# Performance work log

Measured on AMD Instinct MI355X. Metric: run time of the kernel, lower is better.

Reference implementation:

```python
import jax, jax.numpy as jnp
import numpy as np

EPS = 1e-6
HQ, HKV, HD = 16, 4, 64   # num_q_heads, num_kv_heads, head_dim
TOPK = 2                  # num_exp_tokens
B, S, H, E, I = 2, 1024, 1024, 8, 2048


def _rms(x, w):
    return x * jax.lax.rsqrt(jnp.mean(x * x, -1, keepdims=True) + EPS) * w


def _rope(x, cos, sin):
    # x: [B,S,h,D]; cos/sin: [S,D/2]
    x1, x2 = jnp.split(x, 2, axis=-1)
    c = cos[None, :, None, :]
    s = sin[None, :, None, :]
    return jnp.concatenate([x1 * c - x2 * s, x1 * s + x2 * c], axis=-1)


def setup_inputs() -> dict:
    key = jax.random.key(0)
    ks = jax.random.split(key, 12)
    w = lambda k, sh: jax.random.normal(k, sh, jnp.float32) * 0.02
    return {
        "x": jax.random.normal(ks[0], (B, S, H), jnp.float32),
        "freq": jax.random.uniform(ks[1], (S, HD // 2), jnp.float32) * 6.28,
        "norm1_w": jnp.ones((H,), jnp.float32),
        "norm2_w": jnp.ones((H,), jnp.float32),
        "wq": w(ks[2], (H, HQ * HD)),
        "wk": w(ks[3], (H, HKV * HD)),
        "wv": w(ks[4], (H, HKV * HD)),
        "wo": w(ks[5], (HQ * HD, H)),
        "qn_w": jnp.ones((HD,), jnp.float32),
        "kn_w": jnp.ones((HD,), jnp.float32),
        "gate_w": w(ks[6], (H, E)),
        "w1": w(ks[7], (E, H, I)),
        "w2": w(ks[8], (E, I, H)),
        "w3": w(ks[9], (E, H, I)),
    }


def reference(x, freq, norm1_w, norm2_w, wq, wk, wv, wo, qn_w, kn_w,
              gate_w, w1, w2, w3):
    b, s, h = x.shape
    # ---- GQA attention with qk_norm + RoPE ----
    hn = _rms(x, norm1_w)
    q = (hn @ wq).reshape(b, s, HQ, HD)
    k = (hn @ wk).reshape(b, s, HKV, HD)
    v = (hn @ wv).reshape(b, s, HKV, HD)
    q = _rms(q, qn_w)
    k = _rms(k, kn_w)
    cos, sin = jnp.cos(freq), jnp.sin(freq)
    q = _rope(q, cos, sin)
    k = _rope(k, cos, sin)
    rep = HQ // HKV
    kr = jnp.repeat(k, rep, axis=2)  # [b,s,HQ,HD]
    vr = jnp.repeat(v, rep, axis=2)
    scores = jnp.einsum('bqhd,bkhd->bhqk', q, kr) * (HD ** -0.5)
    mask = jnp.tril(jnp.ones((s, s), bool))
    scores = jnp.where(mask, scores, jnp.finfo(scores.dtype).min)
    att = jax.nn.softmax(scores, axis=-1)
    y = jnp.einsum('bhqk,bkhd->bqhd', att, vr).reshape(b, s, HQ * HD) @ wo
    x = x + y

    # ---- Sparse MoE FFN (top-k softmax gate, SwiGLU experts) ----
    t = _rms(x, norm2_w).reshape(b * s, h)
    probs = jax.nn.softmax(t @ gate_w, axis=-1)          # [T,E]
    vals, idx = jax.lax.top_k(probs, TOPK)               # [T,k]
    vals = vals / jnp.sum(vals, -1, keepdims=True)       # renormalize top-k
    T = b * s
    combine = jnp.zeros((T, E), t.dtype).at[
        jnp.arange(T)[:, None], idx].add(vals)           # [T,E]
    u = jnp.einsum('th,ehi->eti', t, w1)
    g = jax.nn.silu(u) * jnp.einsum('th,ehi->eti', t, w3)
    ye = jnp.einsum('eti,eih->eth', g, w2)               # [E,T,H]
    moe = jnp.einsum('eth,te->th', ye, combine).reshape(b, s, h)
    return (x + moe, k, v)
```

## Files before the change

kernel.cpp:

```cpp
#include <hip/hip_runtime.h>
#include <hip/hip_bf16.h>

#define HQn 16
#define HKVn 4
#define HDn 64
#define Bn 2
#define Sn 1024
#define Hn 1024
#define En 8
#define In 2048
#define Tn 2048
#define EPSf 1e-6f

typedef __attribute__((ext_vector_type(8))) short bf16x8;
typedef __attribute__((ext_vector_type(4))) float f32x4;

__device__ __forceinline__ unsigned short f2bf(float f) {
  unsigned u = __float_as_uint(f);
  u += 0x7fffu + ((u >> 16) & 1u);
  return (unsigned short)(u >> 16);
}
__device__ __forceinline__ float bf2f(unsigned short u) {
  return __uint_as_float(((unsigned)u) << 16);
}
__device__ __forceinline__ void gll16(const void* g, void* l) {
  __builtin_amdgcn_global_load_lds(
      (const __attribute__((address_space(1))) void*)g,
      (__attribute__((address_space(3))) void*)l, 16, 0, 0);
}

__global__ __launch_bounds__(256) void k_tcvt(
    const float* __restrict__ src, unsigned short* __restrict__ dst,
    int R, int C, size_t sZ, size_t dZ) {
  src += (size_t)blockIdx.z * sZ;
  dst += (size_t)blockIdx.z * dZ;
  int c0 = blockIdx.x * 64, r0 = blockIdx.y * 64;
  __shared__ float t[64][65];
  int tid = threadIdx.x;
  int lr = tid >> 4, lc = (tid & 15) * 4;
#pragma unroll
  for (int p = 0; p < 4; p++) {
    float4 v = *(const float4*)(src + (size_t)(r0 + lr + p * 16) * C + c0 + lc);
    t[lr + p * 16][lc + 0] = v.x; t[lr + p * 16][lc + 1] = v.y;
    t[lr + p * 16][lc + 2] = v.z; t[lr + p * 16][lc + 3] = v.w;
  }
  __syncthreads();
  int oc = tid >> 2;
  int seg = (tid & 3) * 16;
  unsigned pk[8];
#pragma unroll
  for (int j = 0; j < 8; j++) {
    unsigned short lo = f2bf(t[seg + 2 * j][oc]);
    unsigned short hi = f2bf(t[seg + 2 * j + 1][oc]);
    pk[j] = (unsigned)lo | ((unsigned)hi << 16);
  }
  uint4* dp = (uint4*)(dst + (size_t)(c0 + oc) * R + r0 + seg);
  dp[0] = make_uint4(pk[0], pk[1], pk[2], pk[3]);
  dp[1] = make_uint4(pk[4], pk[5], pk[6], pk[7]);
}

__global__ __launch_bounds__(256) void k_tcvt2(
    const float* __restrict__ src, unsigned short* __restrict__ dsth,
    unsigned short* __restrict__ dstl, int R, int C) {
  int c0 = blockIdx.x * 64, r0 = blockIdx.y * 64;
  __shared__ float t[64][65];
  int tid = threadIdx.x;
  int lr = tid >> 4, lc = (tid & 15) * 4;
#pragma unroll
  for (int p = 0; p < 4; p++) {
    float4 v = *(const float4*)(src + (size_t)(r0 + lr + p * 16) * C + c0 + lc);
    t[lr + p * 16][lc + 0] = v.x; t[lr + p * 16][lc + 1] = v.y;
    t[lr + p * 16][lc + 2] = v.z; t[lr + p * 16][lc + 3] = v.w;
  }
  __syncthreads();
  int oc = tid >> 2;
  int seg = (tid & 3) * 16;
  unsigned pkh[8], pkl[8];
#pragma unroll
  for (int j = 0; j < 8; j++) {
    float a = t[seg + 2 * j][oc], b = t[seg + 2 * j + 1][oc];
    unsigned short ahh = f2bf(a), bhh = f2bf(b);
    unsigned short alo = f2bf(a - bf2f(ahh)), blo = f2bf(b - bf2f(bhh));
    pkh[j] = (unsigned)ahh | ((unsigned)bhh << 16);
    pkl[j] = (unsigned)alo | ((unsigned)blo << 16);
  }
  size_t db = (size_t)(c0 + oc) * R + r0 + seg;
  uint4* dph = (uint4*)(dsth + db);
  dph[0] = make_uint4(pkh[0], pkh[1], pkh[2], pkh[3]);
  dph[1] = make_uint4(pkh[4], pkh[5], pkh[6], pkh[7]);
  uint4* dpl = (uint4*)(dstl + db);
  dpl[0] = make_uint4(pkl[0], pkl[1], pkl[2], pkl[3]);
  dpl[1] = make_uint4(pkl[4], pkl[5], pkl[6], pkl[7]);
}

__global__ __launch_bounds__(256) void k_rmsnorm(
    const float* __restrict__ x, const float* __restrict__ w,
    unsigned short* __restrict__ outh, unsigned short* __restrict__ outl) {
  int row = blockIdx.x, tid = threadIdx.x;
  size_t off = (size_t)row * Hn + tid * 4;
  float4 v = *(const float4*)(x + off);
  float ss = v.x * v.x + v.y * v.y + v.z * v.z + v.w * v.w;
#pragma unroll
  for (int o = 32; o > 0; o >>= 1) ss += __shfl_xor(ss, o);
  __shared__ float ls[4];
  if ((tid & 63) == 0) ls[tid >> 6] = ss;
  __syncthreads();
  float tot = ls[0] + ls[1] + ls[2] + ls[3];
  float sc = rsqrtf(tot * (1.0f / Hn) + EPSf);
  float4 wv = *(const float4*)(w + tid * 4);
  float o0 = v.x * sc * wv.x, o1 = v.y * sc * wv.y;
  float o2 = v.z * sc * wv.z, o3 = v.w * sc * wv.w;
  ushort4 h4, l4;
  h4.x = f2bf(o0); l4.x = f2bf(o0 - bf2f(h4.x));
  h4.y = f2bf(o1); l4.y = f2bf(o1 - bf2f(h4.y));
  h4.z = f2bf(o2); l4.z = f2bf(o2 - bf2f(h4.z));
  h4.w = f2bf(o3); l4.w = f2bf(o3 - bf2f(h4.w));
  *(ushort4*)(outh + off) = h4;
  *(ushort4*)(outl + off) = l4;
}

__global__ __launch_bounds__(256) void k_resid_norm(
    const float* __restrict__ x, const float* __restrict__ y,
    const float* __restrict__ w, float* __restrict__ x2out,
    float* __restrict__ tout, unsigned short* __restrict__ tbf) {
  int row = blockIdx.x, tid = threadIdx.x;
  size_t off = (size_t)row * Hn + tid * 4;
  float4 xv = *(const float4*)(x + off);
  float4 yv = *(const float4*)(y + off);
  float4 s;
  s.x = xv.x + yv.x; s.y = xv.y + yv.y; s.z = xv.z + yv.z; s.w = xv.w + yv.w;
  *(float4*)(x2out + off) = s;
  float ss = s.x * s.x + s.y * s.y + s.z * s.z + s.w * s.w;
#pragma unroll
  for (int o = 32; o > 0; o >>= 1) ss += __shfl_xor(ss, o);
  __shared__ float ls[4];
  if ((tid & 63) == 0) ls[tid >> 6] = ss;
  __syncthreads();
  float tot = ls[0] + ls[1] + ls[2] + ls[3];
  float sc = rsqrtf(tot * (1.0f / Hn) + EPSf);
  float4 wv4 = *(const float4*)(w + tid * 4);
  float4 t4;
  t4.x = s.x * sc * wv4.x; t4.y = s.y * sc * wv4.y;
  t4.z = s.z * sc * wv4.z; t4.w = s.w * sc * wv4.w;
  *(float4*)(tout + off) = t4;
  ushort4 b4;
  b4.x = f2bf(t4.x); b4.y = f2bf(t4.y); b4.z = f2bf(t4.z); b4.w = f2bf(t4.w);
  *(ushort4*)(tbf + off) = b4;
}

template<int MT>
__global__ __launch_bounds__(256) void k_pgemm(
    const unsigned short* __restrict__ Ah, const unsigned short* __restrict__ Al,
    const unsigned short* __restrict__ Bth, const unsigned short* __restrict__ Btl,
    float* __restrict__ C, int N, int K) {
  constexpr int BM = MT * 32;
  constexpr int ASL = BM * 32;
  __shared__ __align__(16) short smAh[2][ASL], smAl[2][ASL];
  __shared__ __align__(16) short smBh[2][4096], smBl[2][4096];
  int tid = threadIdx.x, wave = tid >> 6, lane = tid & 63;
  int n0 = blockIdx.x * 128, m0 = blockIdx.y * BM;
  int wm = wave >> 1, wn = wave & 1;
  int r0 = ((tid >> 6) << 4) | (tid & 15);
  int k0 = ((tid >> 4) & 3) * 8;
  int r1 = r0 + 64;
  const unsigned short* pAh0 = Ah + (size_t)(m0 + r0) * K + k0;
  const unsigned short* pAl0 = Al + (size_t)(m0 + r0) * K + k0;
  const unsigned short* pBh0 = Bth + (size_t)(n0 + r0) * K + k0;
  const unsigned short* pBl0 = Btl + (size_t)(n0 + r0) * K + k0;
  const unsigned short* pBh1 = Bth + (size_t)(n0 + r1) * K + k0;
  const unsigned short* pBl1 = Btl + (size_t)(n0 + r1) * K + k0;
  const unsigned short* pAh1 = pAh0;
  const unsigned short* pAl1 = pAl0;
  if constexpr (MT == 4) {
    pAh1 = Ah + (size_t)(m0 + r1) * K + k0;
    pAl1 = Al + (size_t)(m0 + r1) * K + k0;
  }
  int d0 = tid * 8, d1 = (256 + tid) * 8;
  auto STAGE = [&](int b, int kb) {
    gll16(pAh0 + kb, &smAh[b][d0]);
    gll16(pAl0 + kb, &smAl[b][d0]);
    if constexpr (MT == 4) {
      gll16(pAh1 + kb, &smAh[b][d1]);
      gll16(pAl1 + kb, &smAl[b][d1]);
    }
    gll16(pBh0 + kb, &smBh[b][d0]);
    gll16(pBl0 + kb, &smBl[b][d0]);
    gll16(pBh1 + kb, &smBh[b][d1]);
    gll16(pBl1 + kb, &smBl[b][d1]);
  };
  f32x4 zf = {0.f, 0.f, 0.f, 0.f};
  f32x4 acc[MT][4];
#pragma unroll
  for (int i = 0; i < MT; i++)
#pragma unroll
    for (int j = 0; j < 4; j++) acc[i][j] = zf;
  STAGE(0, 0);
  __syncthreads();
  for (int kb = 0; kb < K; kb += 32) {
    int cur = (kb >> 5) & 1;
    if (kb + 32 < K) STAGE(cur ^ 1, kb + 32);
    bf16x8 ah[MT], al[MT], bh[4], bl[4];
#pragma unroll
    for (int i = 0; i < MT; i++) {
      ah[i] = *(const bf16x8*)&smAh[cur][((wm * MT + i) * 64 + lane) * 8];
      al[i] = *(const bf16x8*)&smAl[cur][((wm * MT + i) * 64 + lane) * 8];
    }
#pragma unroll
    for (int j = 0; j < 4; j++) {
      bh[j] = *(const bf16x8*)&smBh[cur][((wn * 4 + j) * 64 + lane) * 8];
      bl[j] = *(const bf16x8*)&smBl[cur][((wn * 4 + j) * 64 + lane) * 8];
    }
#pragma unroll
    for (int i = 0; i < MT; i++)
#pragma unroll
      for (int j = 0; j < 4; j++) {
        acc[i][j] = __builtin_amdgcn_mfma_f32_16x16x32_bf16(ah[i], bh[j], acc[i][j], 0, 0, 0);
        acc[i][j] = __builtin_amdgcn_mfma_f32_16x16x32_bf16(ah[i], bl[j], acc[i][j], 0, 0, 0);
        acc[i][j] = __builtin_amdgcn_mfma_f32_16x16x32_bf16(al[i], bh[j], acc[i][j], 0, 0, 0);
      }
    __syncthreads();
  }
  int cr = (lane >> 4) * 4, cc = lane & 15;
#pragma unroll
  for (int i = 0; i < MT; i++) {
    int row0 = m0 + (wm * MT + i) * 16 + cr;
#pragma unroll
    for (int j = 0; j < 4; j++) {
      int col = n0 + (wn * 4 + j) * 16 + cc;
#pragma unroll
      for (int r = 0; r < 4; r++)
        C[(size_t)(row0 + r) * N + col] = acc[i][j][r];
    }
  }
}

__global__ __launch_bounds__(256) void k_qkv_post(
    const float* __restrict__ qkv, const float* __restrict__ qn_w,
    const float* __restrict__ kn_w, const float* __restrict__ freq,
    float* __restrict__ q_t,
    unsigned short* __restrict__ kT8h, unsigned short* __restrict__ kT8l,
    unsigned short* __restrict__ vT8h, unsigned short* __restrict__ vT8l,
    float* __restrict__ k_out, float* __restrict__ v_out) {
  int gw = blockIdx.x * 4 + (threadIdx.x >> 6);
  int lane = threadIdx.x & 63;
  int token = gw / 24;
  int hh = gw % 24;
  int b = token / Sn, s = token % Sn;
  if (hh >= 20) {
    int h = hh - 20;
    float v = qkv[(size_t)token * 1536 + 1280 + h * HDn + lane];
    unsigned short hi = f2bf(v);
    unsigned short lo = f2bf(v - bf2f(hi));
    size_t vb = (((size_t)(b * HKVn + h) * 128 + (s >> 3)) * 64 + lane) * 8 + (s & 7);
    vT8h[vb] = hi; vT8l[vb] = lo;
    v_out[(size_t)token * (HKVn * HDn) + h * HDn + lane] = v;
    return;
  }
  bool isq = hh < 16;
  int h = isq ? hh : hh - 16;
  float val = isq ? qkv[(size_t)token * 1536 + h * HDn + lane]
                  : qkv[(size_t)token * 1536 + 1024 + h * HDn + lane];
  float ss = val * val;
#pragma unroll
  for (int o = 32; o > 0; o >>= 1) ss += __shfl_xor(ss, o);
  float scn = rsqrtf(ss * (1.0f / HDn) + EPSf);
  float w = isq ? qn_w[lane] : kn_w[lane];
  float xn = val * scn * w;
  float f = freq[(size_t)s * (HDn / 2) + (lane & 31)];
  float c = cosf(f), sn = sinf(f);
  float partner = __shfl_xor(xn, 32);
  float out = (lane < 32) ? (xn * c - partner * sn) : (partner * sn + xn * c);
  if (isq) {
    q_t[(((size_t)(b * HQn + h)) * Sn + s) * HDn + lane] = out;
  } else {
    unsigned short hi = f2bf(out);
    unsigned short lo = f2bf(out - bf2f(hi));
    size_t kb = (((size_t)(b * HKVn + h) * 8 + (lane >> 3)) * Sn + s) * 8 + (lane & 7);
    kT8h[kb] = hi; kT8l[kb] = lo;
    k_out[(size_t)token * (HKVn * HDn) + h * HDn + lane] = out;
  }
}

__global__ __launch_bounds__(256) void k_attn_mfma(
    const float* __restrict__ q_t,
    const unsigned short* __restrict__ kT8h, const unsigned short* __restrict__ kT8l,
    const unsigned short* __restrict__ vT8h, const unsigned short* __restrict__ vT8l,
    unsigned short* __restrict__ yh, unsigned short* __restrict__ yl) {
  __shared__ __align__(16) unsigned short klh[4096], kll[4096];
  __shared__ __align__(16) unsigned short vth[4096], vtl[4096];
  __shared__ __align__(16) unsigned short Ph[4][1152], Pl[4][1152];
  int bid = blockIdx.x;
  int qt = 63 - (bid & 63);
  int kvh = (bid >> 6) & 3;
  int b = bid >> 8;
  int tid = threadIdx.x, w = tid >> 6, lane = tid & 63;
  int h = kvh * 4 + w;
  int g = lane >> 4, li = lane & 15;
  const float* qrow = q_t + (((size_t)(b * HQn + h) * Sn) + qt * 16 + li) * HDn + g * 8;
  bf16x8 qh[2], ql[2];
#pragma unroll
  for (int kc = 0; kc < 2; kc++) {
    float v[8];
    *(float4*)(v) = *(const float4*)(qrow + kc * 32);
    *(float4*)(v + 4) = *(const float4*)(qrow + kc * 32 + 4);
#pragma unroll
    for (int j = 0; j < 8; j++) {
      unsigned short hi = f2bf(v[j]);
      qh[kc][j] = (short)hi;
      ql[kc][j] = (short)f2bf(v[j] - bf2f(hi));
    }
  }
  size_t bh = (size_t)(b * HKVn + kvh) * 65536;
  f32x4 acc[4];
  f32x4 zf = {0.f, 0.f, 0.f, 0.f};
#pragma unroll
  for (int nt = 0; nt < 4; nt++) acc[nt] = zf;
  float m_[4] = {-1e30f, -1e30f, -1e30f, -1e30f};
  float l_[4] = {0.f, 0.f, 0.f, 0.f};
  int rowb = qt * 16 + g * 4;
  int kmax = qt * 16 + 15;
  for (int kk = 0; kk <= kmax; kk += 64) {
    __syncthreads();
#pragma unroll
    for (int i = 0; i < 2; i++) {
      int idx = w * 2 + i;
      gll16(kT8h + bh + (size_t)idx * 8192 + (size_t)kk * 8 + lane * 8, &klh[idx * 512]);
      gll16(kT8l + bh + (size_t)idx * 8192 + (size_t)kk * 8 + lane * 8, &kll[idx * 512]);
      gll16(vT8h + bh + (size_t)(kk / 8 + idx) * 512 + lane * 8, &vth[idx * 512]);
      gll16(vT8l + bh + (size_t)(kk / 8 + idx) * 512 + lane * 8, &vtl[idx * 512]);
    }
    __syncthreads();
    f32x4 st[4];
#pragma unroll
    for (int kt = 0; kt < 4; kt++) st[kt] = zf;
#pragma unroll
    for (int kt = 0; kt < 4; kt++)
#pragma unroll
      for (int kc = 0; kc < 2; kc++) {
        int ko = (kc * 4 + g) * 512 + (kt * 16 + li) * 8;
        bf16x8 kh = *(const bf16x8*)&klh[ko];
        bf16x8 klo = *(const bf16x8*)&kll[ko];
        st[kt] = __builtin_amdgcn_mfma_f32_16x16x32_bf16(qh[kc], kh, st[kt], 0, 0, 0);
        st[kt] = __builtin_amdgcn_mfma_f32_16x16x32_bf16(qh[kc], klo, st[kt], 0, 0, 0);
        st[kt] = __builtin_amdgcn_mfma_f32_16x16x32_bf16(ql[kc], kh, st[kt], 0, 0, 0);
      }
    float mx[4] = {-1e30f, -1e30f, -1e30f, -1e30f};
#pragma unroll
    for (int kt = 0; kt < 4; kt++) {
      int key = kk + kt * 16 + li;
#pragma unroll
      for (int r = 0; r < 4; r++) {
        float s = st[kt][r] * 0.125f;
        if (key > rowb + r) s = -1e30f;
        st[kt][r] = s;
        mx[r] = fmaxf(mx[r], s);
      }
    }
#pragma unroll
    for (int r = 0; r < 4; r++) {
#pragma unroll
      for (int o = 1; o < 16; o <<= 1) mx[r] = fmaxf(mx[r], __shfl_xor(mx[r], o));
      float mn = fmaxf(m_[r], mx[r]);
      mx[r] = __expf(m_[r] - mn);
      m_[r] = mn;
    }
    float rs[4] = {0.f, 0.f, 0.f, 0.f};
#pragma unroll
    for (int kt = 0; kt < 4; kt++)
#pragma unroll
      for (int r = 0; r < 4; r++) {
        float p = __expf(st[kt][r] - m_[r]);
        rs[r] += p;
        unsigned short phh = f2bf(p);
        Ph[w][(g * 4 + r) * 72 + kt * 16 + li] = phh;
        Pl[w][(g * 4 + r) * 72 + kt * 16 + li] = f2bf(p - bf2f(phh));
      }
#pragma unroll
    for (int r = 0; r < 4; r++) {
#pragma unroll
      for (int o = 1; o < 16; o <<= 1) rs[r] += __shfl_xor(rs[r], o);
      l_[r] = l_[r] * mx[r] + rs[r];
#pragma unroll
      for (int nt = 0; nt < 4; nt++) acc[nt][r] *= mx[r];
    }
    bf16x8 pfh[2], pfl[2];
#pragma unroll
    for (int kc = 0; kc < 2; kc++) {
      int po = li * 72 + kc * 32 + g * 8;
      pfh[kc] = *(const bf16x8*)&Ph[w][po];
      pfl[kc] = *(const bf16x8*)&Pl[w][po];
    }
#pragma unroll
    for (int nt = 0; nt < 4; nt++)
#pragma unroll
      for (int kc = 0; kc < 2; kc++) {
        int vo = (kc * 4 + g) * 512 + (nt * 16 + li) * 8;
        bf16x8 vh = *(const bf16x8*)&vth[vo];
        bf16x8 vl = *(const bf16x8*)&vtl[vo];
        acc[nt] = __builtin_amdgcn_mfma_f32_16x16x32_bf16(pfh[kc], vh, acc[nt], 0, 0, 0);
        acc[nt] = __builtin_amdgcn_mfma_f32_16x16x32_bf16(pfh[kc], vl, acc[nt], 0, 0, 0);
        acc[nt] = __builtin_amdgcn_mfma_f32_16x16x32_bf16(pfl[kc], vh, acc[nt], 0, 0, 0);
      }
  }
  size_t ybase = ((size_t)(b * Sn) + qt * 16) * (HQn * HDn) + h * HDn;
#pragma unroll
  for (int r = 0; r < 4; r++) {
    float inv = 1.f / l_[r];
#pragma unroll
    for (int nt = 0; nt < 4; nt++) {
      size_t idx = ybase + (size_t)(g * 4 + r) * (HQn * HDn) + nt * 16 + li;
      float v = acc[nt][r] * inv;
      unsigned short hi = f2bf(v);
      yh[idx] = hi;
      yl[idx] = f2bf(v - bf2f(hi));
    }
  }
}

__global__ __launch_bounds__(256) void k_router(
    const float* __restrict__ t, const float* __restrict__ gw_,
    int* __restrict__ idx, float* __restrict__ val, int* __restrict__ cnt) {
  int tok = blockIdx.x * 4 + (threadIdx.x >> 6);
  int lane = threadIdx.x & 63;
  const float* tr = t + (size_t)tok * Hn;
  float s[8] = {0, 0, 0, 0, 0, 0, 0, 0};
  for (int hh = lane; hh < Hn; hh += 64) {
    float tv = tr[hh];
    float4 g0 = *(const float4*)(gw_ + hh * 8);
    float4 g1 = *(const float4*)(gw_ + hh * 8 + 4);
    s[0] = fmaf(tv, g0.x, s[0]); s[1] = fmaf(tv, g0.y, s[1]);
    s[2] = fmaf(tv, g0.z, s[2]); s[3] = fmaf(tv, g0.w, s[3]);
    s[4] = fmaf(tv, g1.x, s[4]); s[5] = fmaf(tv, g1.y, s[5]);
    s[6] = fmaf(tv, g1.z, s[6]); s[7] = fmaf(tv, g1.w, s[7]);
  }
#pragma unroll
  for (int e = 0; e < 8; e++)
#pragma unroll
    for (int off = 32; off > 0; off >>= 1) s[e] += __shfl_xor(s[e], off);
  if (lane == 0) {
    float mx = s[0];
    for (int e = 1; e < 8; e++) mx = fmaxf(mx, s[e]);
    float p[8];
    for (int e = 0; e < 8; e++) p[e] = __expf(s[e] - mx);
    int e0 = 0;
    for (int e = 1; e < 8; e++) if (p[e] > p[e0]) e0 = e;
    int e1 = (e0 == 0) ? 1 : 0;
    for (int e = 0; e < 8; e++) if (e != e0 && p[e] > p[e1]) e1 = e;
    float v0 = p[e0], v1 = p[e1], inv = 1.f / (v0 + v1);
    idx[tok * 2] = e0; idx[tok * 2 + 1] = e1;
    val[tok * 2] = v0 * inv; val[tok * 2 + 1] = v1 * inv;
    atomicAdd(&cnt[e0], 1); atomicAdd(&cnt[e1], 1);
  }
}

__global__ void k_scan(const int* __restrict__ cnt, int* __restrict__ offs,
                       int* __restrict__ cursor) {
  if (threadIdx.x == 0) {
    int run = 0;
    for (int e = 0; e < En; e++) { offs[e] = run; cursor[e] = run; run += cnt[e]; }
  }
}

__global__ __launch_bounds__(256) void k_scatter(
    const int* __restrict__ idx, const float* __restrict__ val,
    int* __restrict__ cursor, int* __restrict__ tokl, float* __restrict__ wvl) {
  int t = blockIdx.x * 256 + threadIdx.x;
#pragma unroll
  for (int slot = 0; slot < 2; slot++) {
    int e = idx[t * 2 + slot];
    int pos = atomicAdd(&cursor[e], 1);
    tokl[pos] = t;
    wvl[pos] = val[t * 2 + slot];
  }
}

__global__ __launch_bounds__(256) void k_gather(
    const unsigned short* __restrict__ tb, const int* __restrict__ tokl,
    unsigned short* __restrict__ tg) {
  int r = blockIdx.x;
  int tk = tokl[r];
  const ushort4* s = (const ushort4*)(tb + (size_t)tk * Hn);
  ushort4* d = (ushort4*)(tg + (size_t)r * Hn);
  d[threadIdx.x] = s[threadIdx.x];
}

__global__ __launch_bounds__(512) void k_moe13(
    const unsigned short* __restrict__ tg, const unsigned short* __restrict__ w13t,
    unsigned short* __restrict__ ug, const int* __restrict__ cnt,
    const int* __restrict__ offs) {
  int e = blockIdx.z;
  int n_e = cnt[e];
  int mt = blockIdx.y;
  if (mt * 256 >= n_e) return;
  int base = offs[e];
  const unsigned short* A = tg + (size_t)(base + mt * 256) * Hn;
  const unsigned short* Bt = w13t + (size_t)e * (2 * In) * Hn;
  __shared__ __align__(16) short smA[2][8192];
  __shared__ __align__(16) short smB[2][4096];
  int tid = threadIdx.x;
  int wave = tid >> 6, lane = tid & 63;
  int n0 = blockIdx.x * 128;
  int wm = wave >> 1, wn = wave & 1;
  int r0s = ((tid >> 6) << 4) | (tid & 15);
  int k0s = ((tid >> 4) & 3) * 8;
  const unsigned short* ApA = A + (size_t)r0s * Hn + k0s;
  const unsigned short* ApB = A + (size_t)(r0s + 128) * Hn + k0s;
  const unsigned short* BpB = Bt + (size_t)(n0 + r0s) * Hn + k0s;
  auto STAGE = [&](int b, int kb) {
    gll16(ApA + kb, &smA[b][tid * 8]);
    gll16(ApB + kb, &smA[b][(512 + tid) * 8]);
    gll16(BpB + kb, &smB[b][tid * 8]);
  };
  f32x4 zf = {0.f, 0.f, 0.f, 0.f};
  f32x4 acc[4][4];
#pragma unroll
  for (int i = 0; i < 4; i++)
#pragma unroll
    for (int j = 0; j < 4; j++) acc[i][j] = zf;
  STAGE(0, 0);
  __syncthreads();
  for (int kb = 0; kb < Hn; kb += 32) {
    int cur = (kb >> 5) & 1;
    if (kb + 32 < Hn) STAGE(cur ^ 1, kb + 32);
    bf16x8 af[4], bfr[4];
#pragma unroll
    for (int i = 0; i < 4; i++)
      af[i] = *(const bf16x8*)&smA[cur][((wm * 4 + i) * 64 + lane) * 8];
#pragma unroll
    for (int j = 0; j < 4; j++)
      bfr[j] = *(const bf16x8*)&smB[cur][((wn * 4 + j) * 64 + lane) * 8];
#pragma unroll
    for (int i = 0; i < 4; i++)
#pragma unroll
      for (int j = 0; j < 4; j++)
        acc[i][j] = __builtin_amdgcn_mfma_f32_16x16x32_bf16(af[i], bfr[j], acc[i][j], 0, 0, 0);
    __syncthreads();
  }
  int cr = (lane >> 4) * 4, cc = lane & 15;
#pragma unroll
  for (int i = 0; i < 4; i++) {
    int lrow0 = wm * 64 + i * 16 + cr;
#pragma unroll
    for (int j = 0; j < 4; j++) {
      int ncol = n0 + wn * 64 + j * 16 + cc;
#pragma unroll
      for (int r = 0; r < 4; r++) {
        int rr = mt * 256 + lrow0 + r;
        if (rr < n_e)
          ug[(size_t)(base + rr) * (2 * In) + ncol] = f2bf(acc[i][j][r]);
      }
    }
  }
}

__global__ __launch_bounds__(256) void k_act(
    const unsigned short* __restrict__ ug, unsigned short* __restrict__ act) {
  size_t p = ((size_t)blockIdx.x * 256 + threadIdx.x) * 8;
  size_t r = p >> 11;
  int c = (int)(p & 2047);
  const ushort4* up = (const ushort4*)(ug + r * 4096 + c);
  const ushort4* gp = (const ushort4*)(ug + r * 4096 + 2048 + c);
  ushort4* ap = (ushort4*)(act + r * 2048 + c);
#pragma unroll
  for (int h = 0; h < 2; h++) {
    ushort4 uu = up[h], gg = gp[h];
    ushort4 oo;
    float u0 = bf2f(uu.x), u1 = bf2f(uu.y), u2 = bf2f(uu.z), u3 = bf2f(uu.w);
    oo.x = f2bf(u0 / (1.f + __expf(-u0)) * bf2f(gg.x));
    oo.y = f2bf(u1 / (1.f + __expf(-u1)) * bf2f(gg.y));
    oo.z = f2bf(u2 / (1.f + __expf(-u2)) * bf2f(gg.z));
    oo.w = f2bf(u3 / (1.f + __expf(-u3)) * bf2f(gg.w));
    ap[h] = oo;
  }
}

__global__ __launch_bounds__(512) void k_moe2(
    const unsigned short* __restrict__ act, const unsigned short* __restrict__ w2t,
    const int* __restrict__ cnt, const int* __restrict__ offs,
    const int* __restrict__ tokl, const float* __restrict__ wvl,
    float* __restrict__ out0) {
  int e = blockIdx.z;
  int n_e = cnt[e];
  int mt = blockIdx.y;
  if (mt * 128 >= n_e) return;
  int base = offs[e];
  __shared__ int ltok[128];
  __shared__ float lwv[128];
  int tid = threadIdx.x;
  if (tid < 128) {
    int rr = mt * 128 + tid;
    bool v = rr < n_e;
    ltok[tid] = v ? tokl[base + rr] : -1;
    lwv[tid] = v ? wvl[base + rr] : 0.f;
  }
  const unsigned short* A = act + (size_t)(base + mt * 128) * In;
  const unsigned short* Bt = w2t + (size_t)e * Hn * In;
  __shared__ __align__(16) short smA[2][4096];
  __shared__ __align__(16) short smB[2][4096];
  int wave = tid >> 6, lane = tid & 63;
  int n0 = blockIdx.x * 128;
  int wm = wave >> 1, wn = wave & 1;
  int r0s = ((tid >> 6) << 4) | (tid & 15);
  int k0s = ((tid >> 4) & 3) * 8;
  const unsigned short* ApA = A + (size_t)r0s * In + k0s;
  const unsigned short* BpB = Bt + (size_t)(n0 + r0s) * In + k0s;
  auto STAGE = [&](int b, int kb) {
    gll16(ApA + kb, &smA[b][tid * 8]);
    gll16(BpB + kb, &smB[b][tid * 8]);
  };
  f32x4 zf = {0.f, 0.f, 0.f, 0.f};
  f32x4 acc[2][4];
#pragma unroll
  for (int i = 0; i < 2; i++)
#pragma unroll
    for (int j = 0; j < 4; j++) acc[i][j] = zf;
  STAGE(0, 0);
  __syncthreads();
  for (int kb = 0; kb < In; kb += 32) {
    int cur = (kb >> 5) & 1;
    if (kb + 32 < In) STAGE(cur ^ 1, kb + 32);
    bf16x8 af[2], bfr[4];
#pragma unroll
    for (int i = 0; i < 2; i++)
      af[i] = *(const bf16x8*)&smA[cur][((wm * 2 + i) * 64 + lane) * 8];
#pragma unroll
    for (int j = 0; j < 4; j++)
      bfr[j] = *(const bf16x8*)&smB[cur][((wn * 4 + j) * 64 + lane) * 8];
#pragma unroll
    for (int i = 0; i < 2; i++)
#pragma unroll
      for (int j = 0; j < 4; j++)
        acc[i][j] = __builtin_amdgcn_mfma_f32_16x16x32_bf16(af[i], bfr[j], acc[i][j], 0, 0, 0);
    __syncthreads();
  }
  int cr = (lane >> 4) * 4, cc = lane & 15;
#pragma unroll
  for (int i = 0; i < 2; i++) {
    int lrow0 = wm * 32 + i * 16 + cr;
#pragma unroll
    for (int j = 0; j < 4; j++) {
      int ncol = n0 + wn * 64 + j * 16 + cc;
#pragma unroll
      for (int r = 0; r < 4; r++) {
        int lrow = lrow0 + r;
        int tk = ltok[lrow];
        if (tk >= 0)
          atomicAdd(out0 + (size_t)tk * Hn + ncol, lwv[lrow] * acc[i][j][r]);
      }
    }
  }
}

extern "C" void kernel_launch(void* const* d_in, const int* in_sizes, int n_in,
                              void* d_out, int out_size, void* d_ws, size_t ws_size,
                              hipStream_t stream) {
  (void)in_sizes; (void)n_in; (void)out_size; (void)ws_size;
  const float* x      = (const float*)d_in[0];
  const float* freq   = (const float*)d_in[1];
  const float* n1w    = (const float*)d_in[2];
  const float* n2w    = (const float*)d_in[3];
  const float* wq     = (const float*)d_in[4];
  const float* wk     = (const float*)d_in[5];
  const float* wvp    = (const float*)d_in[6];
  const float* wo     = (const float*)d_in[7];
  const float* qn_w   = (const float*)d_in[8];
  const float* kn_w   = (const float*)d_in[9];
  const float* gate_w = (const float*)d_in[10];
  const float* w1     = (const float*)d_in[11];
  const float* w2     = (const float*)d_in[12];
  const float* w3     = (const float*)d_in[13];

  float* out0  = (float*)d_out;
  float* k_out = out0 + (size_t)Tn * Hn;
  float* v_out = k_out + (size_t)Tn * HKVn * HDn;

  char* wsb = (char*)d_ws;
  unsigned short* w13t = (unsigned short*)(wsb + 0);
  unsigned short* w2t  = (unsigned short*)(wsb + 67108864);
  unsigned short* tbf  = (unsigned short*)(wsb + 100663296);
  unsigned short* tg   = (unsigned short*)(wsb + 104857600);
  unsigned short* wqkvt_h = (unsigned short*)(wsb + 113246208);
  unsigned short* wqkvt_l = (unsigned short*)(wsb + 116391936);
  unsigned short* wot_h   = (unsigned short*)(wsb + 119537664);
  unsigned short* wot_l   = (unsigned short*)(wsb + 121634816);
  unsigned short* act  = (unsigned short*)(wsb + 113246208);
  unsigned short* hnh  = (unsigned short*)(wsb + 130023424);
  unsigned short* hnl  = (unsigned short*)(wsb + 134217728);
  float* qkv_raw = (float*)(wsb + 138412032);
  float* q_t   = (float*)(wsb + 150994944);
  unsigned short* kT8h = (unsigned short*)(wsb + 159383552);
  unsigned short* kT8l = (unsigned short*)(wsb + 160432128);
  unsigned short* vT8h = (unsigned short*)(wsb + 161480704);
  unsigned short* vT8l = (unsigned short*)(wsb + 162529280);
  unsigned short* ug = (unsigned short*)(wsb + 130023424);
  unsigned short* yh = (unsigned short*)(wsb + 163577856);
  unsigned short* yl = (unsigned short*)(wsb + 167772160);
  float* y2    = (float*)(wsb + 171966464);
  float* t_norm = (float*)(wsb + 150994944);
  char*  rtr   = wsb + 180355072;
  int*   idxb   = (int*)(rtr);
  float* valb   = (float*)(rtr + 16384);
  int*   cnt    = (int*)(rtr + 32768);
  int*   offs   = (int*)(rtr + 32768 + 128);
  int*   cursor = (int*)(rtr + 32768 + 256);
  int*   tokl   = (int*)(rtr + 32768 + 384);
  float* wvl    = (float*)(rtr + 32768 + 384 + 16384);

  k_tcvt<<<dim3(32, 16, 8), 256, 0, stream>>>(w1, w13t, 1024, 2048,
                                              (size_t)1024 * 2048, (size_t)4096 * 1024);
  k_tcvt<<<dim3(32, 16, 8), 256, 0, stream>>>(w3, w13t + (size_t)2048 * 1024, 1024, 2048,
                                              (size_t)1024 * 2048, (size_t)4096 * 1024);
  k_tcvt<<<dim3(16, 32, 8), 256, 0, stream>>>(w2, w2t, 2048, 1024,
                                              (size_t)2048 * 1024, (size_t)1024 * 2048);
  k_tcvt2<<<dim3(16, 16), 256, 0, stream>>>(wq, wqkvt_h, wqkvt_l, 1024, 1024);
  k_tcvt2<<<dim3(4, 16), 256, 0, stream>>>(wk, wqkvt_h + (size_t)1024 * 1024,
                                           wqkvt_l + (size_t)1024 * 1024, 1024, 256);
  k_tcvt2<<<dim3(4, 16), 256, 0, stream>>>(wvp, wqkvt_h + (size_t)1280 * 1024,
                                           wqkvt_l + (size_t)1280 * 1024, 1024, 256);
  k_tcvt2<<<dim3(16, 16), 256, 0, stream>>>(wo, wot_h, wot_l, 1024, 1024);

  hipMemsetAsync(cnt, 0, 8 * sizeof(int), stream);

  k_rmsnorm<<<Tn, 256, 0, stream>>>(x, n1w, hnh, hnl);
  k_pgemm<4><<<dim3(12, 16), 256, 0, stream>>>(hnh, hnl, wqkvt_h, wqkvt_l,
                                               qkv_raw, 1536, 1024);
  k_qkv_post<<<(Tn * 24) / 4, 256, 0, stream>>>(qkv_raw, qn_w, kn_w,
                                                freq, q_t, kT8h, kT8l, vT8h, vT8l,
                                                k_out, v_out);
  k_attn_mfma<<<Bn * HKVn * 64, 256, 0, stream>>>(q_t, kT8h, kT8l, vT8h, vT8l, yh, yl);
  k_pgemm<2><<<dim3(8, 32), 256, 0, stream>>>(yh, yl, wot_h, wot_l, y2, 1024, 1024);
  k_resid_norm<<<Tn, 256, 0, stream>>>(x, y2, n2w, out0, t_norm, tbf);
  k_router<<<Tn / 4, 256, 0, stream>>>(t_norm, gate_w, idxb, valb, cnt);
  k_scan<<<1, 64, 0, stream>>>(cnt, offs, cursor);
  k_scatter<<<Tn / 256, 256, 0, stream>>>(idxb, valb, cursor, tokl, wvl);
  k_gather<<<2 * Tn, 256, 0, stream>>>(tbf, tokl, tg);
  k_moe13<<<dim3(32, 8, 8), 512, 0, stream>>>(tg, w13t, ug, cnt, offs);
  k_act<<<4096, 256, 0, stream>>>(ug, act);
  k_moe2<<<dim3(8, 16, 8), 512, 0, stream>>>(act, w2t, cnt, offs, tokl, wvl, out0);
}
```

Measured before the change: 680.6 us.

## Enlarge MoE w1/w3 GEMM tile to 256x256 with K=64 double-buffered stages

The expert up-projection GEMM now computes a 256x256 output tile per block instead of 256x128, with each wave owning 128x64. Each pipeline stage loads 64 K-elements instead of 32, through two named shared buffers, and the grid along N is halved. This raises arithmetic intensity and halves the number of barriers per K step. The cost is 128KB of LDS and 128 accumulator registers per thread, which lowers occupancy, and fewer blocks run when experts get few tokens.

```diff
diff --git a/kernel.cpp b/kernel.cpp
--- a/kernel.cpp
+++ b/kernel.cpp
@@ -493,53 +493,70 @@
   int mt = blockIdx.y;
   if (mt * 256 >= n_e) return;
   int base = offs[e];
+  int n0 = blockIdx.x * 256;
   const unsigned short* A = tg + (size_t)(base + mt * 256) * Hn;
-  const unsigned short* Bt = w13t + (size_t)e * (2 * In) * Hn;
-  __shared__ __align__(16) short smA[2][8192];
-  __shared__ __align__(16) short smB[2][4096];
+  const unsigned short* Bt = w13t + (size_t)e * (2 * In) * Hn + (size_t)n0 * Hn;
+  __shared__ __align__(16) short sA0[16384], sA1[16384];
+  __shared__ __align__(16) short sB0[16384], sB1[16384];
   int tid = threadIdx.x;
   int wave = tid >> 6, lane = tid & 63;
-  int n0 = blockIdx.x * 128;
-  int wm = wave >> 1, wn = wave & 1;
-  int r0s = ((tid >> 6) << 4) | (tid & 15);
-  int k0s = ((tid >> 4) & 3) * 8;
-  const unsigned short* ApA = A + (size_t)r0s * Hn + k0s;
-  const unsigned short* ApB = A + (size_t)(r0s + 128) * Hn + k0s;
-  const unsigned short* BpB = Bt + (size_t)(n0 + r0s) * Hn + k0s;
-  auto STAGE = [&](int b, int kb) {
-    gll16(ApA + kb, &smA[b][tid * 8]);
-    gll16(ApB + kb, &smA[b][(512 + tid) * 8]);
-    gll16(BpB + kb, &smB[b][tid * 8]);
-  };
+  int wm = wave >> 2, wn = wave & 3;
+  int rowLo = ((tid >> 6) << 4) | (tid & 15);
+  int kLo = ((tid >> 4) & 3) * 8;
+  const unsigned short* a0 = A + (size_t)rowLo * Hn + kLo;
+  const unsigned short* a1 = A + (size_t)(rowLo + 128) * Hn + kLo;
+  const unsigned short* b0 = Bt + (size_t)rowLo * Hn + kLo;
+  const unsigned short* b1 = Bt + (size_t)(rowLo + 128) * Hn + kLo;
+  size_t d0 = (size_t)tid * 8;
+#define M13_STAGE(S, kb) do { \
+    gll16(a0 + (kb), sA##S + d0); \
+    gll16(a1 + (kb), sA##S + 4096 + d0); \
+    gll16(a0 + (kb) + 32, sA##S + 8192 + d0); \
+    gll16(a1 + (kb) + 32, sA##S + 12288 + d0); \
+    gll16(b0 + (kb), sB##S + d0); \
+    gll16(b1 + (kb), sB##S + 4096 + d0); \
+    gll16(b0 + (kb) + 32, sB##S + 8192 + d0); \
+    gll16(b1 + (kb) + 32, sB##S + 12288 + d0); \
+  } while (0)
+#define M13_COMP(S) do { \
+    _Pragma("unroll") \
+    for (int kk = 0; kk < 2; kk++) { \
+      bf16x8 af[8], bfr[4]; \
+      _Pragma("unroll") \
+      for (int i = 0; i < 8; i++) \
+        af[i] = *(const bf16x8*)(sA##S + kk * 8192 + ((wm * 8 + i) * 64 + lane) * 8); \
+      _Pragma("unroll") \
+      for (int j = 0; j < 4; j++) \
+        bfr[j] = *(const bf16x8*)(sB##S + kk * 8192 + ((wn * 4 + j) * 64 + lane) * 8); \
+      _Pragma("unroll") \
+      for (int i = 0; i < 8; i++) \
+        _Pragma("unroll") \
+        for (int j = 0; j < 4; j++) \
+          acc[i][j] = __builtin_amdgcn_mfma_f32_16x16x32_bf16(af[i], bfr[j], acc[i][j], 0, 0, 0); \
+    } \
+  } while (0)
   f32x4 zf = {0.f, 0.f, 0.f, 0.f};
-  f32x4 acc[4][4];
-#pragma unroll
-  for (int i = 0; i < 4; i++)
+  f32x4 acc[8][4];
+#pragma unroll
+  for (int i = 0; i < 8; i++)
 #pragma unroll
     for (int j = 0; j < 4; j++) acc[i][j] = zf;
-  STAGE(0, 0);
+  M13_STAGE(0, 0);
   __syncthreads();
-  for (int kb = 0; kb < Hn; kb += 32) {
-    int cur = (kb >> 5) & 1;
-    if (kb + 32 < Hn) STAGE(cur ^ 1, kb + 32);
-    bf16x8 af[4], bfr[4];
-#pragma unroll
-    for (int i = 0; i < 4; i++)
-      af[i] = *(const bf16x8*)&smA[cur][((wm * 4 + i) * 64 + lane) * 8];
-#pragma unroll
-    for (int j = 0; j < 4; j++)
-      bfr[j] = *(const bf16x8*)&smB[cur][((wn * 4 + j) * 64 + lane) * 8];
-#pragma unroll
-    for (int i = 0; i < 4; i++)
-#pragma unroll
-      for (int j = 0; j < 4; j++)
-        acc[i][j] = __builtin_amdgcn_mfma_f32_16x16x32_bf16(af[i], bfr[j], acc[i][j], 0, 0, 0);
+  for (int kb = 0; kb < Hn; kb += 128) {
+    M13_STAGE(1, kb + 64);
+    M13_COMP(0);
     __syncthreads();
-  }
+    if (kb + 128 < Hn) M13_STAGE(0, kb + 128);
+    M13_COMP(1);
+    __syncthreads();
+  }
+#undef M13_STAGE
+#undef M13_COMP
   int cr = (lane >> 4) * 4, cc = lane & 15;
 #pragma unroll
-  for (int i = 0; i < 4; i++) {
-    int lrow0 = wm * 64 + i * 16 + cr;
+  for (int i = 0; i < 8; i++) {
+    int lrow0 = wm * 128 + i * 16 + cr;
 #pragma unroll
     for (int j = 0; j < 4; j++) {
       int ncol = n0 + wn * 64 + j * 16 + cc;
@@ -734,7 +751,7 @@
   k_scan<<<1, 64, 0, stream>>>(cnt, offs, cursor);
   k_scatter<<<Tn / 256, 256, 0, stream>>>(idxb, valb, cursor, tokl, wvl);
   k_gather<<<2 * Tn, 256, 0, stream>>>(tbf, tokl, tg);
-  k_moe13<<<dim3(32, 8, 8), 512, 0, stream>>>(tg, w13t, ug, cnt, offs);
+  k_moe13<<<dim3(16, 8, 8), 512, 0, stream>>>(tg, w13t, ug, cnt, offs);
   k_act<<<4096, 256, 0, stream>>>(ug, act);
   k_moe2<<<dim3(8, 16, 8), 512, 0, stream>>>(act, w2t, cnt, offs, tokl, wvl, out0);
 }
```

Result: no change. 679.5 us (-0.2%).
